# Kernel tuning notes

Measured on AMD Instinct MI355X. Metric: run time of the kernel, lower is better.

Reference implementation:

```python
import jax, jax.numpy as jnp
import numpy as np

N_HEADS = 16
K_CH = 1024 // N_HEADS  # 64
SCALE = 1.0 / np.sqrt(K_CH)


def setup_inputs() -> dict:
    key = jax.random.key(0)
    ks = jax.random.split(key, 10)
    B, C, T = 4, 1024, 2048
    Cout = 1024
    xavier = lambda k, o, i: jax.random.uniform(k, (o, i), jnp.float32, -1.0, 1.0) * np.sqrt(6.0 / (o + i))
    return {
        "x": jax.random.normal(ks[0], (B, C, T), jnp.float32),
        "c": jax.random.normal(ks[1], (B, C, T), jnp.float32),
        "Wq": xavier(ks[2], C, C), "bq": jnp.zeros((C,), jnp.float32),
        "Wk": xavier(ks[3], C, C), "bk": jnp.zeros((C,), jnp.float32),
        "Wv": xavier(ks[4], C, C), "bv": jnp.zeros((C,), jnp.float32),
        "Wo": xavier(ks[5], Cout, C), "bo": jnp.zeros((Cout,), jnp.float32),
    }


def reference(x, c, Wq, bq, Wk, bk, Wv, bv, Wo, bo):
    B, C, T = x.shape
    H, K = N_HEADS, K_CH
    # 1x1 Conv1d == per-timestep linear: [O,C] @ [B,C,T] -> [B,O,T]
    q = jnp.einsum('oc,bct->bot', Wq, x) + bq[None, :, None]
    k = jnp.einsum('oc,bct->bot', Wk, c) + bk[None, :, None]
    v = jnp.einsum('oc,bct->bot', Wv, c) + bv[None, :, None]
    # split heads: b (h k) t -> b h k t
    q = q.reshape(B, H, K, T)
    k = k.reshape(B, H, K, -1)
    v = v.reshape(B, H, K, -1)
    scores = jnp.einsum('bhkt,bhks->bhts', q, k) * SCALE  # [B,H,Tt,Ts]
    p = jax.nn.softmax(scores, axis=-1)
    out = jnp.einsum('bhts,bhks->bhkt', p, v)  # b h k t
    out = out.reshape(B, H * K, T)
    return jnp.einsum('oc,bct->bot', Wo, out) + bo[None, :, None]
```

## Files before the change

kernel.cpp:

```cpp
#include <hip/hip_runtime.h>
#include <stdint.h>

typedef __bf16 bf16x8 __attribute__((ext_vector_type(8)));
typedef float f32x4 __attribute__((ext_vector_type(4)));
typedef float f32x16 __attribute__((ext_vector_type(16)));
typedef unsigned u32x2 __attribute__((ext_vector_type(2)));
typedef unsigned u32x4 __attribute__((ext_vector_type(4)));

#define LOG2E 1.44269504088896340736f
#define ATT_SCALE 0.125f
#define CL (ATT_SCALE * LOG2E)
#define SWZ(row, colb) ((colb) ^ (((row) & 7) << 4))

#define GLOAD_LDS16(gp, lp)                                                  \
  __builtin_amdgcn_global_load_lds(                                          \
      (const __attribute__((address_space(1))) void*)(gp),                   \
      (__attribute__((address_space(3))) void*)(lp), 16, 0, 0)

__device__ __forceinline__ unsigned short f2bf(float f) {
  unsigned int x = __float_as_uint(f);
  x += 0x7fffu + ((x >> 16) & 1u);
  return (unsigned short)(x >> 16);
}

__device__ __forceinline__ float fexp2(float x) {
#if __has_builtin(__builtin_amdgcn_exp2f)
  return __builtin_amdgcn_exp2f(x);
#else
  return exp2f(x);
#endif
}

__device__ __forceinline__ unsigned cvtpk(float lo, float hi) {
  unsigned r;
  asm("v_cvt_pk_bf16_f32 %0, %1, %2" : "=v"(r) : "v"(lo), "v"(hi));
  return r;
}

__device__ __forceinline__ u32x2 plswap(unsigned a, unsigned b) {
  asm("v_permlane32_swap_b32 %0, %1" : "+v"(a), "+v"(b));
  u32x2 r;
  r[0] = a;
  r[1] = b;
  return r;
}

__global__ __launch_bounds__(256) void cvt_weights(
    const float* __restrict__ w0, const float* __restrict__ w1,
    const float* __restrict__ w2, const float* __restrict__ w3,
    unsigned short* __restrict__ o0, unsigned short* __restrict__ o1,
    unsigned short* __restrict__ o2, unsigned short* __restrict__ o3) {
  int sel = blockIdx.x >> 10;
  const float* in = sel == 0 ? w0 : sel == 1 ? w1 : sel == 2 ? w2 : w3;
  unsigned short* out = sel == 0 ? o0 : sel == 1 ? o1 : sel == 2 ? o2 : o3;
  float scale = sel == 0 ? CL : 1.0f;
  int i = ((blockIdx.x & 1023) * 256 + threadIdx.x) * 4;
  float4 v = *(const float4*)(in + i);
  ushort4 o;
  o.x = f2bf(v.x * scale); o.y = f2bf(v.y * scale);
  o.z = f2bf(v.z * scale); o.w = f2bf(v.w * scale);
  *(ushort4*)(out + i) = o;
}

__global__ __launch_bounds__(256) void transpose_cvt2(const float* __restrict__ x,
                                                      const float* __restrict__ c,
                                                      unsigned short* __restrict__ xT,
                                                      unsigned short* __restrict__ cT) {
  __shared__ unsigned short tile[32][33];
  const int C = 1024, T = 2048;
  int z = blockIdx.z;
  const float* in = (z < 4) ? x : c;
  unsigned short* out = (z < 4) ? xT : cT;
  int b = z & 3;
  int t0 = blockIdx.x * 32, c0 = blockIdx.y * 32;
  int tx = threadIdx.x & 31, ty = threadIdx.x >> 5;
  const float* src = in + ((size_t)b * C + c0) * T + t0;
  #pragma unroll
  for (int i = 0; i < 4; ++i) {
    int cc = ty + i * 8;
    tile[cc][tx] = f2bf(src[(size_t)cc * T + tx]);
  }
  __syncthreads();
  unsigned short* dst = out + ((size_t)b * T + t0) * C + c0;
  #pragma unroll
  for (int i = 0; i < 4; ++i) {
    int tt = ty + i * 8;
    dst[(size_t)tt * C + tx] = tile[tx][tt];
  }
}

template <int NT, int OUT_F32>
__device__ __forceinline__ void gemm_core128(
    const unsigned short* __restrict__ A, const unsigned short* __restrict__ B,
    void* __restrict__ Cv, const float* __restrict__ bias, int bias_is_m,
    float bs, int m0, int n0, int ldC) {
  __shared__ __align__(16) char lds[3 * 16384];
  const int tid = threadIdx.x;
  const int l = tid & 63, w = tid >> 6;
  const int g = l >> 4, j = l & 15;
  const int wr = w >> 1, wc = w & 1;

  const int r0 = tid >> 3;
  const int slotp = (tid & 7) ^ (r0 & 7);
  const int mloc = r0 * 2 + (slotp >> 2);
  const int kg = slotp & 3;
  const unsigned short* ga0 = A + (size_t)(m0 + mloc) * 1024 + kg * 8;
  const unsigned short* ga1 = A + (size_t)(m0 + 64 + mloc) * 1024 + kg * 8;
  const unsigned short* gb0 = B + (size_t)(n0 + mloc) * 1024 + kg * 8;
  const unsigned short* gb1 = B + (size_t)(n0 + 64 + mloc) * 1024 + kg * 8;

  auto stage = [&](char* buf) {
    GLOAD_LDS16(ga0, buf + tid * 16);
    GLOAD_LDS16(ga1, buf + 4096 + tid * 16);
    GLOAD_LDS16(gb0, buf + 8192 + tid * 16);
    GLOAD_LDS16(gb1, buf + 12288 + tid * 16);
    ga0 += 32; ga1 += 32; gb0 += 32; gb1 += 32;
  };

  f32x4 acc[4][4] = {};

  stage(lds);
  stage(lds + 16384);

  char* bufc = lds;
  char* bufs = lds + 2 * 16384;

  for (int t = 0; t < NT; ++t) {
    if (t == NT - 1) asm volatile("s_waitcnt vmcnt(0)" ::: "memory");
    else             asm volatile("s_waitcnt vmcnt(4)" ::: "memory");
    __builtin_amdgcn_s_barrier();
    asm volatile("" ::: "memory");
    if (t < NT - 2) stage(bufs);

    bf16x8 af[4], bfr[4];
    #pragma unroll
    for (int mf = 0; mf < 4; ++mf) {
      int m = wr * 64 + mf * 16 + j;
      int rp = m >> 1;
      int cb = ((m & 1) * 64 + g * 16) ^ ((rp & 7) << 4);
      af[mf] = *(const bf16x8*)(bufc + rp * 128 + cb);
    }
    #pragma unroll
    for (int nf = 0; nf < 4; ++nf) {
      int n = wc * 64 + nf * 16 + j;
      int rp = n >> 1;
      int cb = ((n & 1) * 64 + g * 16) ^ ((rp & 7) << 4);
      bfr[nf] = *(const bf16x8*)(bufc + 8192 + rp * 128 + cb);
    }
    #pragma unroll
    for (int mf = 0; mf < 4; ++mf)
      #pragma unroll
      for (int nf = 0; nf < 4; ++nf)
        acc[mf][nf] = __builtin_amdgcn_mfma_f32_16x16x32_bf16(af[mf], bfr[nf], acc[mf][nf], 0, 0, 0);

    bufc += 16384; if (bufc == lds + 49152) bufc = lds;
    bufs += 16384; if (bufs == lds + 49152) bufs = lds;
  }

  #pragma unroll
  for (int mf = 0; mf < 4; ++mf) {
    #pragma unroll
    for (int rr = 0; rr < 4; ++rr) {
      int m = m0 + wr * 64 + mf * 16 + g * 4 + rr;
      float bm = bias_is_m ? bias[m] * bs : 0.f;
      #pragma unroll
      for (int nf = 0; nf < 4; ++nf) {
        int n = n0 + wc * 64 + nf * 16 + j;
        float val = acc[mf][nf][rr] + bm + (bias_is_m ? 0.f : bias[n] * bs);
        if (OUT_F32) ((float*)Cv)[(size_t)m * ldC + n] = val;
        else ((unsigned short*)Cv)[(size_t)m * ldC + n] = f2bf(val);
      }
    }
  }
}

__global__ __launch_bounds__(256, 3) void qkv_gemm3(
    const unsigned short* __restrict__ xT, const unsigned short* __restrict__ cT,
    const unsigned short* __restrict__ wq, const unsigned short* __restrict__ wk,
    const unsigned short* __restrict__ wv,
    const float* __restrict__ bq, const float* __restrict__ bk,
    const float* __restrict__ bv,
    unsigned short* __restrict__ QT, unsigned short* __restrict__ KT,
    unsigned short* __restrict__ Vb) {
  const size_t sBT = (size_t)2048 * 1024;
  const int id = (blockIdx.x & 7) * 192 + (blockIdx.x >> 3);
  const int op = id >> 9;
  const int r = id & 511;
  const int z = r >> 7;
  const unsigned short *A, *B;
  unsigned short* Cp;
  const float* bias;
  int m0, n0, ldC, bias_is_m;
  float bs;
  if (op == 2) {
    n0 = (r & 15) * 128; m0 = ((r >> 4) & 7) * 128;
    A = wv; B = cT + z * sBT; Cp = Vb + z * (size_t)1024 * 2048;
    bias = bv; ldC = 2048; bias_is_m = 1; bs = 1.0f;
  } else {
    n0 = (r & 7) * 128; m0 = ((r >> 3) & 15) * 128;
    A = (op == 0 ? xT : cT) + z * sBT;
    B = (op == 0 ? wq : wk);
    Cp = (op == 0 ? QT : KT) + z * sBT;
    bias = (op == 0 ? bq : bk); ldC = 1024; bias_is_m = 0;
    bs = (op == 0) ? CL : 1.0f;
  }
  gemm_core128<32, 0>(A, B, Cp, bias, bias_is_m, bs, m0, n0, ldC);
}

__global__ __launch_bounds__(256, 3) void gemm_out3(
    const unsigned short* __restrict__ Wo, const unsigned short* __restrict__ OT,
    float* __restrict__ Out, const float* __restrict__ bias) {
  const size_t sBT = (size_t)2048 * 1024;
  const int id = (blockIdx.x & 7) * 64 + (blockIdx.x >> 3);
  const int z = id >> 7;
  const int m0 = ((id >> 4) & 7) * 128, n0 = (id & 15) * 128;
  gemm_core128<32, 1>(Wo, OT + z * sBT, Out + z * (size_t)1024 * 2048,
                      bias, 1, 1.0f, m0, n0, 2048);
}

__global__ __launch_bounds__(256, 4) void attn_kernel5(const unsigned short* __restrict__ QT,
                                                       const unsigned short* __restrict__ KT,
                                                       const unsigned short* __restrict__ V,
                                                       unsigned short* __restrict__ OT) {
  __shared__ __align__(16) char kv[2][16384];

  const int fid = blockIdx.x;
  const int xcd = fid & 7, idx = fid >> 3;
  const int bh = ((idx & 7) << 3) | xcd;
  const int tblk = idx >> 3;
  const int b = bh >> 4, h = bh & 15;

  const int tid = threadIdx.x;
  const int w = tid >> 6, l = tid & 63, lo5 = l & 31, hi = l >> 5;
  const int tq0 = tblk * 128 + w * 32;

  bf16x8 q[4];
  {
    const unsigned short* Qb = QT + ((size_t)(b * 2048 + tq0 + lo5)) * 1024 + h * 64 + hi * 8;
    #pragma unroll
    for (int kb = 0; kb < 4; ++kb) q[kb] = *(const bf16x8*)(Qb + kb * 16);
  }

  f32x16 o[2] = {};
  f32x16 ol = {};

  const unsigned one2 = 0x3F803F80u;
  const bf16x8 ones = __builtin_bit_cast(bf16x8, (u32x4){one2, one2, one2, one2});

  const int srow0 = tid >> 3, sslot = tid & 7;
  const unsigned short* Kg0 = KT + ((size_t)b * 2048) * 1024 + h * 64;
  const unsigned short* Vg0 = V + ((size_t)(b * 1024 + h * 64)) * 2048;

  auto stage = [&](int bsel, int s0) {
    char* Ks = kv[bsel];
    char* Vs = kv[bsel] + 8192;
    #pragma unroll
    for (int p = 0; p < 2; ++p) {
      int row = p * 32 + srow0;
      int ch = sslot ^ (row & 7);
      GLOAD_LDS16(Kg0 + (size_t)(s0 + row) * 1024 + ch * 8, Ks + (p * 256 + tid) * 16);
      GLOAD_LDS16(Vg0 + (size_t)row * 2048 + s0 + ch * 8, Vs + (p * 256 + tid) * 16);
    }
  };

  stage(0, 0);
  __syncthreads();

  for (int t = 0; t < 32; ++t) {
    int cur = t & 1;
    if (t < 31) stage(cur ^ 1, (t + 1) * 64);
    char* Ks = kv[cur];
    char* Vs = kv[cur] + 8192;

    f32x16 p0 = {}, p1 = {};
    #pragma unroll
    for (int kb = 0; kb < 4; ++kb) {
      int r0 = lo5, r1 = 32 + lo5;
      bf16x8 ka0 = *(const bf16x8*)(Ks + r0 * 128 + SWZ(r0, kb * 32 + hi * 16));
      bf16x8 ka1 = *(const bf16x8*)(Ks + r1 * 128 + SWZ(r1, kb * 32 + hi * 16));
      p0 = __builtin_amdgcn_mfma_f32_32x32x16_bf16(ka0, q[kb], p0, 0, 0, 0);
      p1 = __builtin_amdgcn_mfma_f32_32x32x16_bf16(ka1, q[kb], p1, 0, 0, 0);
    }

    #pragma unroll
    for (int r = 0; r < 16; ++r) p0[r] = fexp2(p0[r]);
    #pragma unroll
    for (int r = 0; r < 16; ++r) p1[r] = fexp2(p1[r]);

    u32x4 pa[4];
    {
      u32x2 ra = plswap(cvtpk(p0[0], p0[1]), cvtpk(p0[4], p0[5]));
      u32x2 rb = plswap(cvtpk(p0[2], p0[3]), cvtpk(p0[6], p0[7]));
      pa[0] = (u32x4){ra[0], rb[0], ra[1], rb[1]};
      u32x2 rc = plswap(cvtpk(p0[8], p0[9]), cvtpk(p0[12], p0[13]));
      u32x2 rd = plswap(cvtpk(p0[10], p0[11]), cvtpk(p0[14], p0[15]));
      pa[1] = (u32x4){rc[0], rd[0], rc[1], rd[1]};
      u32x2 re = plswap(cvtpk(p1[0], p1[1]), cvtpk(p1[4], p1[5]));
      u32x2 rf = plswap(cvtpk(p1[2], p1[3]), cvtpk(p1[6], p1[7]));
      pa[2] = (u32x4){re[0], rf[0], re[1], rf[1]};
      u32x2 rg = plswap(cvtpk(p1[8], p1[9]), cvtpk(p1[12], p1[13]));
      u32x2 rh = plswap(cvtpk(p1[10], p1[11]), cvtpk(p1[14], p1[15]));
      pa[3] = (u32x4){rg[0], rh[0], rg[1], rh[1]};
    }

    #pragma unroll
    for (int sb = 0; sb < 4; ++sb) {
      bf16x8 pab = __builtin_bit_cast(bf16x8, pa[sb]);
      #pragma unroll
      for (int kb2 = 0; kb2 < 2; ++kb2) {
        int row = kb2 * 32 + lo5;
        bf16x8 vb = *(const bf16x8*)(Vs + row * 128 + SWZ(row, sb * 32 + hi * 16));
        o[kb2] = __builtin_amdgcn_mfma_f32_32x32x16_bf16(pab, vb, o[kb2], 0, 0, 0);
      }
      ol = __builtin_amdgcn_mfma_f32_32x32x16_bf16(pab, ones, ol, 0, 0, 0);
    }
    __syncthreads();
  }

  unsigned short* Ob = OT + ((size_t)(b * 2048 + tq0)) * 1024 + h * 64 + lo5;
  #pragma unroll
  for (int r = 0; r < 16; ++r) {
    int srow = (r & 3) + 8 * (r >> 2) + 4 * hi;
    float inv = 1.0f / ol[r];
    Ob[(size_t)srow * 1024 + 0]  = f2bf(o[0][r] * inv);
    Ob[(size_t)srow * 1024 + 32] = f2bf(o[1][r] * inv);
  }
}

extern "C" void kernel_launch(void* const* d_in, const int* in_sizes, int n_in,
                              void* d_out, int out_size, void* d_ws, size_t ws_size,
                              hipStream_t stream) {
  const float* x  = (const float*)d_in[0];
  const float* c  = (const float*)d_in[1];
  const float* Wq = (const float*)d_in[2];
  const float* bq = (const float*)d_in[3];
  const float* Wk = (const float*)d_in[4];
  const float* bk = (const float*)d_in[5];
  const float* Wv = (const float*)d_in[6];
  const float* bv = (const float*)d_in[7];
  const float* Wo = (const float*)d_in[8];
  const float* bo = (const float*)d_in[9];

  const size_t MB = 1024 * 1024;
  char* ws = (char*)d_ws;
  unsigned short* wqb = (unsigned short*)(ws + 0 * MB);
  unsigned short* wkb = (unsigned short*)(ws + 2 * MB);
  unsigned short* wvb = (unsigned short*)(ws + 4 * MB);
  unsigned short* wob = (unsigned short*)(ws + 6 * MB);
  unsigned short* xT  = (unsigned short*)(ws + 8 * MB);
  unsigned short* cT  = (unsigned short*)(ws + 24 * MB);
  unsigned short* QT  = (unsigned short*)(ws + 40 * MB);
  unsigned short* KT  = (unsigned short*)(ws + 56 * MB);
  unsigned short* Vb  = (unsigned short*)(ws + 72 * MB);
  unsigned short* OT  = xT;

  cvt_weights<<<dim3(4096), 256, 0, stream>>>(Wq, Wk, Wv, Wo, wqb, wkb, wvb, wob);
  transpose_cvt2<<<dim3(64, 32, 8), 256, 0, stream>>>(x, c, xT, cT);

  qkv_gemm3<<<dim3(1536), 256, 0, stream>>>(xT, cT, wqb, wkb, wvb, bq, bk, bv, QT, KT, Vb);

  attn_kernel5<<<dim3(1024), 256, 0, stream>>>(QT, KT, Vb, OT);

  gemm_out3<<<dim3(512), 256, 0, stream>>>(wob, OT, (float*)d_out, bo);
}
```

Measured before the change: 189.6 us.

## Replace QKV projection GEMM with 256x256-tile, 8-wave pipelined kernel

The fused Q/K/V projection kernel moves from 128x128 tiles (256 threads, three blocks per CU) to 256x256 tiles with 512 threads and one block per CU. It streams 64-wide K slices into double-buffered 128 KB LDS through direct global-to-LDS loads, and interleaves quarter-tile loads with MFMA phases separated by barriers, with raised wave priority during the MFMA bursts. The goal is more operand reuse per byte loaded and better overlap of memory traffic with matrix math. The cost is lower occupancy, a 384-block grid that may load-balance unevenly across CUs, and extra barriers per iteration.

```diff
diff --git a/kernel.cpp b/kernel.cpp
--- a/kernel.cpp
+++ b/kernel.cpp
@@ -16,6 +16,13 @@
   __builtin_amdgcn_global_load_lds(                                          \
       (const __attribute__((address_space(1))) void*)(gp),                   \
       (__attribute__((address_space(3))) void*)(lp), 16, 0, 0)
+
+#define BAR()                                                                \
+  do {                                                                       \
+    asm volatile("" ::: "memory");                                           \
+    __builtin_amdgcn_s_barrier();                                            \
+    asm volatile("" ::: "memory");                                           \
+  } while (0)
 
 __device__ __forceinline__ unsigned short f2bf(float f) {
   unsigned int x = __float_as_uint(f);
@@ -89,6 +96,173 @@
   }
 }
 
+__global__ __launch_bounds__(512, 1) void qkv_gemm256(
+    const unsigned short* __restrict__ xT, const unsigned short* __restrict__ cT,
+    const unsigned short* __restrict__ wq, const unsigned short* __restrict__ wk,
+    const unsigned short* __restrict__ wv,
+    const float* __restrict__ bq, const float* __restrict__ bk,
+    const float* __restrict__ bv,
+    unsigned short* __restrict__ QT, unsigned short* __restrict__ KT,
+    unsigned short* __restrict__ Vb) {
+  __shared__ __align__(16) char lds[131072];
+  const size_t sBT = (size_t)2048 * 1024;
+
+  const int bid = blockIdx.x;
+  const int id = (bid & 7) * 48 + (bid >> 3);
+  const int op = id >> 7;
+  const int r = id & 127;
+  const int z = r >> 5, tt5 = r & 31;
+
+  const unsigned short *Aop, *Bop;
+  unsigned short* Cp;
+  const float* bias;
+  int m0, n0, ldC, bias_is_m;
+  float bs;
+  if (op == 2) {
+    m0 = (tt5 & 3) * 256; n0 = (tt5 >> 2) * 256;
+    Aop = wv; Bop = cT + z * sBT; Cp = Vb + z * (size_t)1024 * 2048;
+    bias = bv; ldC = 2048; bias_is_m = 1; bs = 1.0f;
+  } else {
+    m0 = (tt5 >> 2) * 256; n0 = (tt5 & 3) * 256;
+    Aop = (op == 0 ? xT : cT) + z * sBT;
+    Bop = (op == 0 ? wq : wk);
+    Cp = (op == 0 ? QT : KT) + z * sBT;
+    bias = (op == 0 ? bq : bk); ldC = 1024; bias_is_m = 0;
+    bs = (op == 0) ? CL : 1.0f;
+  }
+
+  const int tid = threadIdx.x;
+  const int l = tid & 63, w = tid >> 6;
+  const int g = l >> 4, j = l & 15;
+  const int wr = w >> 2, wc = w & 3;
+
+  const int lr1 = tid >> 3, lr2 = (tid + 512) >> 3;
+  const int kg1 = (tid & 7) ^ (lr1 & 7), kg2 = (tid & 7) ^ (lr2 & 7);
+  const unsigned short* Pq[4][2];
+  Pq[0][0] = Bop + (size_t)(n0 + lr1) * 1024 + kg1 * 8;
+  Pq[0][1] = Bop + (size_t)(n0 + lr2) * 1024 + kg2 * 8;
+  Pq[1][0] = Bop + (size_t)(n0 + 128 + lr1) * 1024 + kg1 * 8;
+  Pq[1][1] = Bop + (size_t)(n0 + 128 + lr2) * 1024 + kg2 * 8;
+  Pq[2][0] = Aop + (size_t)(m0 + lr1) * 1024 + kg1 * 8;
+  Pq[2][1] = Aop + (size_t)(m0 + lr2) * 1024 + kg2 * 8;
+  Pq[3][0] = Aop + (size_t)(m0 + 128 + lr1) * 1024 + kg1 * 8;
+  Pq[3][1] = Aop + (size_t)(m0 + 128 + lr2) * 1024 + kg2 * 8;
+
+#define STAGE(q, ttile)                                                      \
+  do {                                                                       \
+    char* d_ = lds + (((ttile) & 1) * 65536) + (q) * 16384;                  \
+    GLOAD_LDS16(Pq[q][0] + (ttile) * 64, d_ + tid * 16);                     \
+    GLOAD_LDS16(Pq[q][1] + (ttile) * 64, d_ + 8192 + tid * 16);              \
+  } while (0)
+
+  f32x4 acc[8][4] = {};
+  bf16x8 af[4][2], bfr[4][2];
+
+  STAGE(0, 0); STAGE(1, 0); STAGE(2, 0); STAGE(3, 0); STAGE(0, 1); STAGE(1, 1);
+  asm volatile("s_waitcnt vmcnt(4)" ::: "memory");
+  BAR();
+
+  for (int t = 0; t < 16; ++t) {
+    const char* bc = lds + (t & 1) * 65536;
+    const char* Ab = bc + 32768 + wr * 16384;
+    const char* Bb = bc + (wc >> 1) * 16384;
+    const int Blr = (wc & 1) * 64;
+
+    #pragma unroll
+    for (int mf = 0; mf < 4; ++mf) {
+      int lr = mf * 16 + j;
+      af[mf][0] = *(const bf16x8*)(Ab + lr * 128 + SWZ(lr, g * 16));
+      af[mf][1] = *(const bf16x8*)(Ab + lr * 128 + SWZ(lr, 64 + g * 16));
+    }
+    #pragma unroll
+    for (int nf = 0; nf < 2; ++nf) {
+      int lr = Blr + nf * 16 + j;
+      bfr[nf][0] = *(const bf16x8*)(Bb + lr * 128 + SWZ(lr, g * 16));
+      bfr[nf][1] = *(const bf16x8*)(Bb + lr * 128 + SWZ(lr, 64 + g * 16));
+    }
+    if (t < 15) STAGE(2, t + 1);
+    BAR();
+    __builtin_amdgcn_s_setprio(1);
+    #pragma unroll
+    for (int mf = 0; mf < 4; ++mf)
+      #pragma unroll
+      for (int nf = 0; nf < 2; ++nf)
+        #pragma unroll
+        for (int k2 = 0; k2 < 2; ++k2)
+          acc[mf][nf] = __builtin_amdgcn_mfma_f32_16x16x32_bf16(af[mf][k2], bfr[nf][k2], acc[mf][nf], 0, 0, 0);
+    __builtin_amdgcn_s_setprio(0);
+    BAR();
+
+    #pragma unroll
+    for (int nf = 2; nf < 4; ++nf) {
+      int lr = Blr + nf * 16 + j;
+      bfr[nf][0] = *(const bf16x8*)(Bb + lr * 128 + SWZ(lr, g * 16));
+      bfr[nf][1] = *(const bf16x8*)(Bb + lr * 128 + SWZ(lr, 64 + g * 16));
+    }
+    if (t < 15) STAGE(3, t + 1);
+    BAR();
+    __builtin_amdgcn_s_setprio(1);
+    #pragma unroll
+    for (int mf = 0; mf < 4; ++mf)
+      #pragma unroll
+      for (int nf = 2; nf < 4; ++nf)
+        #pragma unroll
+        for (int k2 = 0; k2 < 2; ++k2)
+          acc[mf][nf] = __builtin_amdgcn_mfma_f32_16x16x32_bf16(af[mf][k2], bfr[nf][k2], acc[mf][nf], 0, 0, 0);
+    __builtin_amdgcn_s_setprio(0);
+    BAR();
+
+    #pragma unroll
+    for (int mf = 0; mf < 4; ++mf) {
+      int lr = (mf + 4) * 16 + j;
+      af[mf][0] = *(const bf16x8*)(Ab + lr * 128 + SWZ(lr, g * 16));
+      af[mf][1] = *(const bf16x8*)(Ab + lr * 128 + SWZ(lr, 64 + g * 16));
+    }
+    if (t < 14) STAGE(0, t + 2);
+    BAR();
+    __builtin_amdgcn_s_setprio(1);
+    #pragma unroll
+    for (int mf = 0; mf < 4; ++mf)
+      #pragma unroll
+      for (int nf = 0; nf < 2; ++nf)
+        #pragma unroll
+        for (int k2 = 0; k2 < 2; ++k2)
+          acc[mf + 4][nf] = __builtin_amdgcn_mfma_f32_16x16x32_bf16(af[mf][k2], bfr[nf][k2], acc[mf + 4][nf], 0, 0, 0);
+    __builtin_amdgcn_s_setprio(0);
+    BAR();
+
+    if (t < 14) STAGE(1, t + 2);
+    __builtin_amdgcn_s_setprio(1);
+    #pragma unroll
+    for (int mf = 0; mf < 4; ++mf)
+      #pragma unroll
+      for (int nf = 2; nf < 4; ++nf)
+        #pragma unroll
+        for (int k2 = 0; k2 < 2; ++k2)
+          acc[mf + 4][nf] = __builtin_amdgcn_mfma_f32_16x16x32_bf16(af[mf][k2], bfr[nf][k2], acc[mf + 4][nf], 0, 0, 0);
+    __builtin_amdgcn_s_setprio(0);
+    if (t == 14) asm volatile("s_waitcnt vmcnt(0)" ::: "memory");
+    else         asm volatile("s_waitcnt vmcnt(4)" ::: "memory");
+    BAR();
+  }
+
+  #pragma unroll
+  for (int mf = 0; mf < 8; ++mf) {
+    #pragma unroll
+    for (int rr = 0; rr < 4; ++rr) {
+      int m = m0 + wr * 128 + mf * 16 + g * 4 + rr;
+      float bm = bias_is_m ? bias[m] * bs : 0.f;
+      #pragma unroll
+      for (int nf = 0; nf < 4; ++nf) {
+        int n = n0 + wc * 64 + nf * 16 + j;
+        float val = acc[mf][nf][rr] + bm + (bias_is_m ? 0.f : bias[n] * bs);
+        Cp[(size_t)m * ldC + n] = f2bf(val);
+      }
+    }
+  }
+#undef STAGE
+}
+
 template <int NT, int OUT_F32>
 __device__ __forceinline__ void gemm_core128(
     const unsigned short* __restrict__ A, const unsigned short* __restrict__ B,
@@ -172,39 +346,6 @@
       }
     }
   }
-}
-
-__global__ __launch_bounds__(256, 3) void qkv_gemm3(
-    const unsigned short* __restrict__ xT, const unsigned short* __restrict__ cT,
-    const unsigned short* __restrict__ wq, const unsigned short* __restrict__ wk,
-    const unsigned short* __restrict__ wv,
-    const float* __restrict__ bq, const float* __restrict__ bk,
-    const float* __restrict__ bv,
-    unsigned short* __restrict__ QT, unsigned short* __restrict__ KT,
-    unsigned short* __restrict__ Vb) {
-  const size_t sBT = (size_t)2048 * 1024;
-  const int id = (blockIdx.x & 7) * 192 + (blockIdx.x >> 3);
-  const int op = id >> 9;
-  const int r = id & 511;
-  const int z = r >> 7;
-  const unsigned short *A, *B;
-  unsigned short* Cp;
-  const float* bias;
-  int m0, n0, ldC, bias_is_m;
-  float bs;
-  if (op == 2) {
-    n0 = (r & 15) * 128; m0 = ((r >> 4) & 7) * 128;
-    A = wv; B = cT + z * sBT; Cp = Vb + z * (size_t)1024 * 2048;
-    bias = bv; ldC = 2048; bias_is_m = 1; bs = 1.0f;
-  } else {
-    n0 = (r & 7) * 128; m0 = ((r >> 3) & 15) * 128;
-    A = (op == 0 ? xT : cT) + z * sBT;
-    B = (op == 0 ? wq : wk);
-    Cp = (op == 0 ? QT : KT) + z * sBT;
-    bias = (op == 0 ? bq : bk); ldC = 1024; bias_is_m = 0;
-    bs = (op == 0) ? CL : 1.0f;
-  }
-  gemm_core128<32, 0>(A, B, Cp, bias, bias_is_m, bs, m0, n0, ldC);
 }
 
 __global__ __launch_bounds__(256, 3) void gemm_out3(
@@ -357,7 +498,7 @@
   cvt_weights<<<dim3(4096), 256, 0, stream>>>(Wq, Wk, Wv, Wo, wqb, wkb, wvb, wob);
   transpose_cvt2<<<dim3(64, 32, 8), 256, 0, stream>>>(x, c, xT, cT);
 
-  qkv_gemm3<<<dim3(1536), 256, 0, stream>>>(xT, cT, wqb, wkb, wvb, bq, bk, bv, QT, KT, Vb);
+  qkv_gemm256<<<dim3(384), 512, 0, stream>>>(xT, cT, wqb, wkb, wvb, bq, bk, bv, QT, KT, Vb);
 
   attn_kernel5<<<dim3(1024), 256, 0, stream>>>(QT, KT, Vb, OT);
 
```

After: 206.3 us. 1.09x slower.
